# Performance work log

Hardware: AMD Instinct MI355X
Metric: run time of the kernel (lower is better)

## Reference

```python
import jax, jax.numpy as jnp
import numpy as np
from jax import lax

HEADS, HEAD_DIM, DIM, DIM_OUT, EPS = 12, 64, 768, 768, 1e-5
REL_DIM = 2 * 56 - 1  # 2*max(q_size, kv_size) - 1


def setup_inputs():
    key = jax.random.key(0)
    ks = jax.random.split(key, 10)
    B, T, H, W = 4, 1, 56, 56
    N = 1 + T * H * W
    s = 0.02
    return {
        "x": jax.random.normal(ks[0], (B, N, DIM), jnp.float32),
        "Wqkv": jax.random.normal(ks[1], (DIM, 3 * DIM_OUT), jnp.float32) * s,
        "pool_q_w": jax.random.normal(ks[2], (HEAD_DIM, 1, 3, 3), jnp.float32) * 0.1,
        "pool_k_w": jax.random.normal(ks[3], (HEAD_DIM, 1, 3, 3), jnp.float32) * 0.1,
        "pool_v_w": jax.random.normal(ks[4], (HEAD_DIM, 1, 3, 3), jnp.float32) * 0.1,
        "gq": jnp.ones((HEAD_DIM,), jnp.float32), "bq": jnp.zeros((HEAD_DIM,), jnp.float32),
        "gk": jnp.ones((HEAD_DIM,), jnp.float32), "bk": jnp.zeros((HEAD_DIM,), jnp.float32),
        "gv": jnp.ones((HEAD_DIM,), jnp.float32), "bv": jnp.zeros((HEAD_DIM,), jnp.float32),
        "rel_pos_h": jax.random.normal(ks[5], (REL_DIM, HEAD_DIM), jnp.float32) * s,
        "rel_pos_w": jax.random.normal(ks[6], (REL_DIM, HEAD_DIM), jnp.float32) * s,
        "Wproj": jax.random.normal(ks[7], (DIM_OUT, DIM_OUT), jnp.float32) * s,
        "bproj": jnp.zeros((DIM_OUT,), jnp.float32),
        "T": 1, "H": 56, "W": 56,
    }


def _layernorm(y, g, b):
    mu = y.mean(-1, keepdims=True)
    var = ((y - mu) ** 2).mean(-1, keepdims=True)
    return (y - mu) * lax.rsqrt(var + EPS) * g + b


def _pool(t, w, stride, g, b, B, H, W):
    # t: (B, heads, 1 + H*W, head_dim). Split cls, depthwise conv over spatial body.
    cls, body = t[:, :, :1], t[:, :, 1:]
    y = body.reshape(B * HEADS, H, W, HEAD_DIM).transpose(0, 3, 1, 2)  # (BH, C, H, W)
    y = lax.conv_general_dilated(y, w, (stride, stride), [(1, 1), (1, 1)],
                                 feature_group_count=HEAD_DIM,
                                 dimension_numbers=("NCHW", "OIHW", "NCHW"))
    Ho, Wo = y.shape[2], y.shape[3]
    y = y.reshape(B, HEADS, HEAD_DIM, Ho * Wo).transpose(0, 1, 3, 2)
    y = jnp.concatenate([cls, y], axis=2)
    return _layernorm(y, g, b), Ho, Wo


def _forward(x, Wqkv, pool_q_w, pool_k_w, pool_v_w, gq, bq, gk, bk, gv, bv,
             rel_pos_h, rel_pos_w, Wproj, bproj, T, H, W):
    B, N, _ = x.shape
    scale = HEAD_DIM ** -0.5
    qkv = (x @ Wqkv).reshape(B, N, 3, HEADS, HEAD_DIM).transpose(2, 0, 3, 1, 4)
    q, k, v = qkv[0], qkv[1], qkv[2]  # (B, heads, N, head_dim)
    q, q_h, q_w = _pool(q, pool_q_w, 1, gq, bq, B, H, W)
    k, k_h, k_w = _pool(k, pool_k_w, 2, gk, bk, B, H, W)
    v, _, _ = _pool(v, pool_v_w, 2, gv, bv, B, H, W)
    attn = jnp.einsum("bhqd,bhkd->bhqk", q * scale, k)
    # relative position bias; index tables are static (shapes known at trace time)
    dh = (np.arange(q_h)[:, None] * max(k_h / q_h, 1.0)
          - np.arange(k_h)[None, :] * max(q_h / k_h, 1.0)
          + (k_h - 1) * max(q_h / k_h, 1.0)).astype(np.int32)
    dw = (np.arange(q_w)[:, None] * max(k_w / q_w, 1.0)
          - np.arange(k_w)[None, :] * max(q_w / k_w, 1.0)
          + (k_w - 1) * max(q_w / k_w, 1.0)).astype(np.int32)
    Rh, Rw = rel_pos_h[dh], rel_pos_w[dw]  # (q_h, k_h, c), (q_w, k_w, c)
    r_q = q[:, :, 1:].reshape(B, HEADS, q_h, q_w, HEAD_DIM)
    rel_h = jnp.einsum("byhwc,hkc->byhwk", r_q, Rh)
    rel_w = jnp.einsum("byhwc,wkc->byhwk", r_q, Rw)
    body = (attn[:, :, 1:, 1:].reshape(B, HEADS, q_h, q_w, k_h, k_w)
            + rel_h[..., None] + rel_w[..., None, :])
    attn = attn.at[:, :, 1:, 1:].set(body.reshape(B, HEADS, q_h * q_w, k_h * k_w))
    attn = jax.nn.softmax(attn, axis=-1)
    out = attn @ v
    out = out.at[:, :, 1:, :].add(q[:, :, 1:, :])  # residual pooling (skips cls)
    out = out.transpose(0, 2, 1, 3).reshape(B, -1, DIM_OUT)
    return out @ Wproj + bproj


def reference(x, Wqkv, pool_q_w, pool_k_w, pool_v_w, gq, bq, gk, bk, gv, bv,
              rel_pos_h, rel_pos_w, Wproj, bproj, T, H, W):
    return _forward(x, Wqkv, pool_q_w, pool_k_w, pool_v_w, gq, bq, gk, bk, gv, bv,
                    rel_pos_h, rel_pos_w, Wproj, bproj, T, H, W)
```

## Files before the change

kernel.cpp:

```cpp
#include <hip/hip_runtime.h>
#include <hip/hip_bf16.h>

#define BATCH 4
#define NTOK 3137
#define DIM 768
#define NHEAD 12
#define HD 64
#define QH 56
#define QW 56
#define NKEY 785
#define NKEYPAD 800
#define THREE_DIM 2304
#define MROWS (BATCH*NTOK)
#define QTILE 64
#define NQT 50
#define NBH 48
#define RELROWS (NBH*56)
#define XD 128

typedef __attribute__((ext_vector_type(8))) short bf16x8;
typedef __attribute__((ext_vector_type(4))) float f32x4;

__device__ __forceinline__ unsigned short f2bf(float f) {
    union { float f; unsigned u; } v; v.f = f;
    unsigned r = v.u + 0x7FFFu + ((v.u >> 16) & 1u);
    return (unsigned short)(r >> 16);
}
__device__ __forceinline__ float bf2f(unsigned short s) {
    union { unsigned u; float f; } v; v.u = (unsigned)s << 16; return v.f;
}
__device__ __forceinline__ int swz64(int x) { return x ^ (((x >> 6) & 7) << 4); }

__device__ __forceinline__ void gl16(const void* g, void* l) {
    __builtin_amdgcn_global_load_lds(
        (const __attribute__((address_space(1))) unsigned int*)g,
        (__attribute__((address_space(3))) unsigned int*)l, 16, 0, 0);
}

__global__ __launch_bounds__(256) void cvt_bf16(
    const float* __restrict__ in, unsigned short* __restrict__ outp, int n4)
{
    for (int i = blockIdx.x * 256 + threadIdx.x; i < n4; i += gridDim.x * 256) {
        float4 v = reinterpret_cast<const float4*>(in)[i];
        union { unsigned short s[4]; uint2 u; } o;
        o.s[0] = f2bf(v.x); o.s[1] = f2bf(v.y);
        o.s[2] = f2bf(v.z); o.s[3] = f2bf(v.w);
        reinterpret_cast<uint2*>(outp)[i] = o.u;
    }
}

__global__ __launch_bounds__(256) void cvt_rel(
    const float* __restrict__ h, const float* __restrict__ w,
    unsigned short* __restrict__ hb, unsigned short* __restrict__ wb)
{
    int i = blockIdx.x * 256 + threadIdx.x;
    const float* src; unsigned short* dst; int j;
    if (i < 1776)      { src = h; dst = hb; j = i; }
    else if (i < 3552) { src = w; dst = wb; j = i - 1776; }
    else return;
    float4 v = reinterpret_cast<const float4*>(src)[j];
    union { unsigned short s[4]; uint2 u; } o;
    o.s[0] = f2bf(v.x); o.s[1] = f2bf(v.y);
    o.s[2] = f2bf(v.z); o.s[3] = f2bf(v.w);
    reinterpret_cast<uint2*>(dst)[j] = o.u;
}

__global__ __launch_bounds__(256) void transpose_bf16_2(
    const float* __restrict__ W0, unsigned short* __restrict__ Wt0,
    const float* __restrict__ W1, unsigned short* __restrict__ Wt1)
{
    const float* W; unsigned short* Wt; int N;
    if (blockIdx.z == 0) { W = W0; Wt = Wt0; N = THREE_DIM; }
    else {
        if (blockIdx.x >= DIM / 32) return;
        W = W1; Wt = Wt1; N = DIM;
    }
    const int K = DIM;
    __shared__ float tile[32][33];
    int k0 = blockIdx.y * 32, n0 = blockIdx.x * 32;
    int t = threadIdx.x;
    int r = t >> 5, c = t & 31;
    #pragma unroll
    for (int p = 0; p < 4; ++p)
        tile[r + p * 8][c] = W[(size_t)(k0 + r + p * 8) * N + n0 + c];
    __syncthreads();
    #pragma unroll
    for (int p = 0; p < 4; ++p)
        Wt[(size_t)(n0 + r + p * 8) * K + k0 + c] = f2bf(tile[c][r + p * 8]);
}

__global__ __launch_bounds__(256) void gemm_mfma(
    const unsigned short* __restrict__ A, const unsigned short* __restrict__ Bt,
    const float* __restrict__ bias, void* __restrict__ C,
    int M, int N, int K, int out_bf16)
{
    __shared__ __align__(16) char lds[32768];
    int t = threadIdx.x;
    int wave = t >> 6, lane = t & 63;
    int lm = lane & 15, lkg = lane >> 4;
    int wr = wave >> 1, wc = wave & 1;

    int gx = gridDim.x;
    int nwg = gx * gridDim.y;
    int lin = blockIdx.y * gx + blockIdx.x;
    int qq = nwg >> 3, rr = nwg & 7;
    int xcd = lin & 7, idx = lin >> 3;
    int newlin = (xcd < rr ? xcd * (qq + 1) : rr * (qq + 1) + (xcd - rr) * qq) + idx;
    int m0 = (newlin / gx) * 128, n0 = (newlin % gx) * 128;

    int o0 = wave * 2048 + lane * 16;
    int o1 = o0 + 1024;
    int r0 = o0 >> 6, s0 = ((o0 >> 4) & 3) ^ ((r0 >> 1) & 3);
    int r1 = o1 >> 6, s1 = ((o1 >> 4) & 3) ^ ((r1 >> 1) & 3);
    int ar0 = m0 + r0; if (ar0 >= M) ar0 = M - 1;
    int ar1 = m0 + r1; if (ar1 >= M) ar1 = M - 1;

    const unsigned short* ap0 = A + (size_t)ar0 * K + s0 * 8;
    const unsigned short* ap1 = A + (size_t)ar1 * K + s1 * 8;
    const unsigned short* bp0 = Bt + (size_t)(n0 + r0) * K + s0 * 8;
    const unsigned short* bp1 = Bt + (size_t)(n0 + r1) * K + s1 * 8;

    int oa0 = o0, oa1 = o1, ob0 = 8192 + o0, ob1 = 8192 + o1;

    f32x4 acc[4][4] = {};
    const int nt = K >> 5;

    gl16(ap0, &lds[oa0]); gl16(ap1, &lds[oa1]);
    gl16(bp0, &lds[ob0]); gl16(bp1, &lds[ob1]);
    ap0 += 32; ap1 += 32; bp0 += 32; bp1 += 32;

    for (int tt = 0; tt < nt; ++tt) {
        int cb = (tt & 1) << 14;
        if (tt + 1 < nt) {
            int nb2 = cb ^ 16384;
            gl16(ap0, &lds[nb2 + oa0]); gl16(ap1, &lds[nb2 + oa1]);
            gl16(bp0, &lds[nb2 + ob0]); gl16(bp1, &lds[nb2 + ob1]);
            ap0 += 32; ap1 += 32; bp0 += 32; bp1 += 32;
            asm volatile("s_waitcnt vmcnt(4)" ::: "memory");
        } else {
            asm volatile("s_waitcnt vmcnt(0)" ::: "memory");
        }
        __builtin_amdgcn_s_barrier();

        bf16x8 af[4], bfr[4];
        #pragma unroll
        for (int m = 0; m < 4; ++m) {
            int row = wr * 64 + m * 16 + lm;
            af[m] = *reinterpret_cast<const bf16x8*>(
                &lds[cb + row * 64 + ((lkg ^ ((row >> 1) & 3)) << 4)]);
        }
        #pragma unroll
        for (int n = 0; n < 4; ++n) {
            int row = wc * 64 + n * 16 + lm;
            bfr[n] = *reinterpret_cast<const bf16x8*>(
                &lds[cb + 8192 + row * 64 + ((lkg ^ ((row >> 1) & 3)) << 4)]);
        }
        #pragma unroll
        for (int m = 0; m < 4; ++m)
            #pragma unroll
            for (int n = 0; n < 4; ++n)
                acc[m][n] = __builtin_amdgcn_mfma_f32_16x16x32_bf16(
                    af[m], bfr[n], acc[m][n], 0, 0, 0);
        __builtin_amdgcn_s_barrier();
    }

    #pragma unroll
    for (int n = 0; n < 4; ++n) {
        int col = n0 + wc * 64 + n * 16 + lm;
        float bval = bias ? bias[col] : 0.f;
        #pragma unroll
        for (int m = 0; m < 4; ++m) {
            int row = m0 + wr * 64 + m * 16 + lkg * 4;
            #pragma unroll
            for (int r = 0; r < 4; ++r) {
                if (row + r < M) {
                    float o = acc[m][n][r] + bval;
                    if (out_bf16)
                        ((unsigned short*)C)[(size_t)(row + r) * N + col] = f2bf(o);
                    else
                        ((float*)C)[(size_t)(row + r) * N + col] = o;
                }
            }
        }
    }
}

__global__ __launch_bounds__(256) void pool_ln_rows(
    const unsigned short* __restrict__ qkvb, const float* __restrict__ w,
    const float* __restrict__ g, const float* __restrict__ beta,
    unsigned short* __restrict__ outp, int qi, int stride, int OH, int OW,
    int mode)
{
    __shared__ unsigned short ibuf[3 * 56 * 64];
    int bid = blockIdx.x;
    int orow = bid % OH;
    int bh = bid / OH;
    int head = bh % NHEAD, b = bh / NHEAD;
    int t = threadIdx.x;
    int wave = t >> 6, lane = t & 63;

    const unsigned short* src =
        qkvb + (size_t)b * NTOK * THREE_DIM + (size_t)qi * DIM + (size_t)head * HD;

    for (int i = t; i < 3 * 56 * 32; i += 256) {
        int pair = i >> 5, off = i & 31;
        int r = pair / 56, iw = pair % 56;
        int ih = orow * stride + r - 1;
        unsigned v = 0;
        if (ih >= 0 && ih < QH)
            v = *reinterpret_cast<const unsigned*>(
                src + (size_t)(1 + ih * QW + iw) * THREE_DIM + off * 2);
        *reinterpret_cast<unsigned*>(&ibuf[pair * 64 + off * 2]) = v;
    }

    float wreg[9];
    #pragma unroll
    for (int k = 0; k < 9; ++k) wreg[k] = w[lane * 9 + k];
    float gl = g[lane], bl = beta[lane];
    __syncthreads();

    int ntask = OW + ((orow == 0) ? 1 : 0);
    for (int task = wave; task < ntask; task += 4) {
        float val;
        int pos;
        if (task == OW) {
            val = bf2f(src[lane]);
            pos = 0;
        } else {
            int ow = task;
            float acc = 0.f;
            #pragma unroll
            for (int r = 0; r < 3; ++r) {
                #pragma unroll
                for (int c = 0; c < 3; ++c) {
                    int iwc = ow * stride + c - 1;
                    if (iwc < 0 || iwc >= QW) continue;
                    acc += bf2f(ibuf[(r * 56 + iwc) * 64 + lane]) * wreg[r * 3 + c];
                }
            }
            val = acc;
            pos = 1 + orow * OW + ow;
        }

        float mu = val;
        #pragma unroll
        for (int off = 32; off > 0; off >>= 1) mu += __shfl_xor(mu, off, 64);
        mu *= (1.f / 64.f);
        float dv = val - mu;
        float var = dv * dv;
        #pragma unroll
        for (int off = 32; off > 0; off >>= 1) var += __shfl_xor(var, off, 64);
        var *= (1.f / 64.f);
        float o = dv * rsqrtf(var + 1e-5f) * gl + bl;

        if (mode == 3) {
            unsigned short* row = outp + ((size_t)bh * NTOK + pos) * XD;
            row[lane] = f2bf(o * 0.125f);
            row[64 + lane] = (lane == 56) ? f2bf(-30.f) : 0;
        } else if (mode == 1) {
            unsigned short* row = outp + ((size_t)bh * NKEYPAD + pos) * XD;
            row[lane] = f2bf(o);
            unsigned short ext = 0;
            if (pos > 0) {
                int kh = (pos - 1) / 28, kw = (pos - 1) % 28;
                if ((lane < 28 && lane == kh) ||
                    (lane >= 28 && lane < 56 && lane - 28 == kw))
                    ext = 0x3F80;
            }
            row[64 + lane] = ext;
        } else {
            outp[((size_t)bh * HD + lane) * NKEYPAD + pos] = f2bf(o);
        }
    }
}

__global__ __launch_bounds__(64) void pad_kv(
    unsigned short* __restrict__ kpx, unsigned short* __restrict__ vt16)
{
    int bh = blockIdx.x;
    int t = threadIdx.x;
    for (int pos = NKEY; pos < NKEYPAD; ++pos) {
        unsigned short* row = kpx + ((size_t)bh * NKEYPAD + pos) * XD;
        row[t] = 0;
        row[64 + t] = (t == 56) ? 0x3F80 : 0;
        vt16[((size_t)bh * HD + t) * NKEYPAD + pos] = 0;
    }
}

__global__ __launch_bounds__(256) void rel_mfma(
    const unsigned short* __restrict__ qpx, const unsigned short* __restrict__ rtab,
    unsigned short* __restrict__ qpx_out, int mode)
{
    __shared__ char bbuf[4096];
    int X = blockIdx.x;
    int m0 = blockIdx.y * 256;
    int t = threadIdx.x;
    int wave = t >> 6, lane = t & 63;
    int lm = lane & 15, lkg = lane >> 4;

    {
        int row = t >> 3, c8 = t & 7;
        int4 val = {0, 0, 0, 0};
        if (row < 28) {
            int dh = X - 2 * row + 54;
            val = *reinterpret_cast<const int4*>(rtab + (size_t)dh * HD + c8 * 8);
        }
        *reinterpret_cast<int4*>(&bbuf[row * 128 + ((c8 * 16) ^ ((row & 7) << 4))]) = val;
    }
    __syncthreads();

    int rbase = m0 + wave * 64 + lm;
    f32x4 acc[4][2] = {};
    #pragma unroll
    for (int kc = 0; kc < 2; ++kc) {
        bf16x8 bfrag[2];
        #pragma unroll
        for (int nb = 0; nb < 2; ++nb) {
            int row = nb * 16 + lm;
            bfrag[nb] = *reinterpret_cast<const bf16x8*>(
                &bbuf[row * 128 + (((kc * 4 + lkg) * 16) ^ ((row & 7) << 4))]);
        }
        #pragma unroll
        for (int m = 0; m < 4; ++m) {
            int rho = rbase + m * 16; if (rho > RELROWS - 1) rho = RELROWS - 1;
            int bh = rho / 56, rem = rho % 56;
            int pos1 = (mode == 0) ? X * 56 + rem : rem * 56 + X;
            const unsigned short* qsrc =
                qpx + ((size_t)bh * NTOK + 1 + pos1) * XD + kc * 32 + lkg * 8;
            bf16x8 af = *reinterpret_cast<const bf16x8*>(qsrc);
            acc[m][0] = __builtin_amdgcn_mfma_f32_16x16x32_bf16(af, bfrag[0], acc[m][0], 0, 0, 0);
            acc[m][1] = __builtin_amdgcn_mfma_f32_16x16x32_bf16(af, bfrag[1], acc[m][1], 0, 0, 0);
        }
    }

    #pragma unroll
    for (int m = 0; m < 4; ++m) {
        #pragma unroll
        for (int r = 0; r < 4; ++r) {
            int rho = m0 + wave * 64 + m * 16 + lkg * 4 + r;
            if (rho >= RELROWS) continue;
            int bh = rho / 56, rem = rho % 56;
            int pos1 = (mode == 0) ? X * 56 + rem : rem * 56 + X;
            unsigned short* dst =
                qpx_out + ((size_t)bh * NTOK + 1 + pos1) * XD + 64 + mode * 28;
            dst[lm] = f2bf(acc[m][0][r] * 8.f);
            if (lm < 12) dst[16 + lm] = f2bf(acc[m][1][r] * 8.f);
        }
    }
}

__global__ __launch_bounds__(256) void attn_mfma(
    const unsigned short* __restrict__ qpx, const unsigned short* __restrict__ kpx,
    const unsigned short* __restrict__ vt, unsigned short* __restrict__ outp)
{
    __shared__ __align__(16) char kbuf[2][8192];
    __shared__ __align__(16) char vbuf[2][4096];
    __shared__ __align__(16) char pbuf[4][1024];

    int bid0 = blockIdx.x;
    int bid = (bid0 & 7) * ((NBH * NQT) / 8) + (bid0 >> 3);
    int tile = bid % NQT;
    int bh = bid / NQT;
    int head = bh % NHEAD, b = bh / NHEAD;
    int q0 = tile * QTILE;
    int t = threadIdx.x;
    int wave = t >> 6, lane = t & 63;
    int lm = lane & 15, lkg = lane >> 4;

    const unsigned short* kb  = kpx + (size_t)bh * NKEYPAD * XD;
    const unsigned short* vtb = vt + (size_t)bh * HD * NKEYPAD;

    bf16x8 qf[4] = {};
    int qrow = q0 + wave * 16 + lm;
    if (qrow < NTOK) {
        const unsigned short* qs = qpx + ((size_t)bh * NTOK + qrow) * XD + lkg * 8;
        qf[0] = *reinterpret_cast<const bf16x8*>(qs);
        qf[1] = *reinterpret_cast<const bf16x8*>(qs + 32);
        qf[2] = *reinterpret_cast<const bf16x8*>(qs + 64);
        qf[3] = *reinterpret_cast<const bf16x8*>(qs + 96);
    }

    f32x4 oacc[4] = {};
    float osum[4] = {0.f, 0.f, 0.f, 0.f};

    int kr0 = t >> 4;
    int ks0 = (t & 15) ^ (kr0 & 7);
    int kr1 = kr0 + 16;
    const unsigned short* kp0 = kb + (size_t)kr0 * XD + ks0 * 8;
    const unsigned short* kp1 = kb + (size_t)kr1 * XD + ks0 * 8;
    int vr = t >> 2;
    int vs = (t & 3) ^ ((vr >> 1) & 3);
    const unsigned short* vp0 = vtb + (size_t)vr * NKEYPAD + vs * 8;
    int kd0 = wave * 1024, kd1 = 4096 + wave * 1024, vd = wave * 1024;

    const int NT = NKEYPAD / 32;

    gl16(kp0, &kbuf[0][kd0]); gl16(kp1, &kbuf[0][kd1]); gl16(vp0, &vbuf[0][vd]);
    kp0 += 32 * XD; kp1 += 32 * XD; vp0 += 32;

    for (int jt = 0; jt < NT; ++jt) {
        int cur = jt & 1;
        if (jt + 1 < NT) {
            gl16(kp0, &kbuf[cur ^ 1][kd0]);
            gl16(kp1, &kbuf[cur ^ 1][kd1]);
            gl16(vp0, &vbuf[cur ^ 1][vd]);
            kp0 += 32 * XD; kp1 += 32 * XD; vp0 += 32;
            asm volatile("s_waitcnt vmcnt(3)" ::: "memory");
        } else {
            asm volatile("s_waitcnt vmcnt(0)" ::: "memory");
        }
        __builtin_amdgcn_s_barrier();

        f32x4 acc0 = {0.f, 0.f, 0.f, 0.f}, acc1 = {0.f, 0.f, 0.f, 0.f};
        #pragma unroll
        for (int kc = 0; kc < 4; ++kc) {
            int sl = (kc * 4 + lkg) ^ (lm & 7);
            bf16x8 kf0 = *reinterpret_cast<const bf16x8*>(&kbuf[cur][lm * 256 + sl * 16]);
            acc0 = __builtin_amdgcn_mfma_f32_16x16x32_bf16(qf[kc], kf0, acc0, 0, 0, 0);
            bf16x8 kf1 = *reinterpret_cast<const bf16x8*>(&kbuf[cur][(16 + lm) * 256 + sl * 16]);
            acc1 = __builtin_amdgcn_mfma_f32_16x16x32_bf16(qf[kc], kf1, acc1, 0, 0, 0);
        }

        #pragma unroll
        for (int nb = 0; nb < 2; ++nb) {
            f32x4 a = nb ? acc1 : acc0;
            #pragma unroll
            for (int r = 0; r < 4; ++r) {
                float e = __expf(a[r]);
                osum[r] += e;
                int baddr = (lkg * 4 + r) * 64 + (nb * 16 + lm) * 2;
                *reinterpret_cast<unsigned short*>(&pbuf[wave][swz64(baddr)]) = f2bf(e);
            }
        }

        bf16x8 pf = *reinterpret_cast<const bf16x8*>(&pbuf[wave][swz64(lm * 64 + lkg * 16)]);
        #pragma unroll
        for (int db = 0; db < 4; ++db) {
            int row = db * 16 + lm;
            bf16x8 vf = *reinterpret_cast<const bf16x8*>(
                &vbuf[cur][row * 64 + ((lkg ^ ((row >> 1) & 3)) << 4)]);
            oacc[db] = __builtin_amdgcn_mfma_f32_16x16x32_bf16(pf, vf, oacc[db], 0, 0, 0);
        }

        __builtin_amdgcn_s_barrier();
    }

    #pragma unroll
    for (int r = 0; r < 4; ++r) {
        float s = osum[r];
        s += __shfl_xor(s, 1, 64);
        s += __shfl_xor(s, 2, 64);
        s += __shfl_xor(s, 4, 64);
        s += __shfl_xor(s, 8, 64);
        osum[r] = 1.f / s;
    }
    #pragma unroll
    for (int r = 0; r < 4; ++r) {
        int qpos = q0 + wave * 16 + lkg * 4 + r;
        if (qpos >= NTOK) continue;
        unsigned short* orow = outp + ((size_t)b * NTOK + qpos) * DIM + (size_t)head * HD;
        const unsigned short* qres = qpx + ((size_t)bh * NTOK + qpos) * XD;
        #pragma unroll
        for (int db = 0; db < 4; ++db) {
            int d = db * 16 + lm;
            float o = oacc[db][r] * osum[r];
            if (qpos > 0) o += bf2f(qres[d]) * 8.f;
            orow[d] = f2bf(o);
        }
    }
}

extern "C" void kernel_launch(void* const* d_in, const int* in_sizes, int n_in,
                              void* d_out, int out_size, void* d_ws, size_t ws_size,
                              hipStream_t stream) {
    const float* x     = (const float*)d_in[0];
    const float* Wqkv  = (const float*)d_in[1];
    const float* pqw   = (const float*)d_in[2];
    const float* pkw   = (const float*)d_in[3];
    const float* pvw   = (const float*)d_in[4];
    const float* gq    = (const float*)d_in[5];
    const float* bq    = (const float*)d_in[6];
    const float* gk    = (const float*)d_in[7];
    const float* bk    = (const float*)d_in[8];
    const float* gv    = (const float*)d_in[9];
    const float* bv    = (const float*)d_in[10];
    const float* rph   = (const float*)d_in[11];
    const float* rpw   = (const float*)d_in[12];
    const float* Wproj = (const float*)d_in[13];
    const float* bproj = (const float*)d_in[14];

    unsigned short* qkvb  = (unsigned short*)d_ws;
    unsigned short* qpx   = qkvb + (size_t)MROWS * THREE_DIM;
    unsigned short* kpx   = qpx + (size_t)NBH * NTOK * XD;
    unsigned short* vt16  = kpx + (size_t)NBH * NKEYPAD * XD;
    unsigned short* xbf   = vt16 + (size_t)NBH * HD * NKEYPAD;
    unsigned short* wqkvt = xbf + (size_t)MROWS * DIM;
    unsigned short* wprojt= wqkvt + (size_t)DIM * THREE_DIM;
    unsigned short* rphb  = wprojt + (size_t)DIM * DIM;
    unsigned short* rpwb  = rphb + 7104;
    unsigned short* attn_bf = qkvb;

    dim3 blk(256);

    cvt_bf16<<<2048, blk, 0, stream>>>(x, xbf, (int)((size_t)MROWS * DIM / 4));
    {
        dim3 g(THREE_DIM / 32, DIM / 32, 2);
        transpose_bf16_2<<<g, blk, 0, stream>>>(Wqkv, wqkvt, Wproj, wprojt);
    }
    cvt_rel<<<14, blk, 0, stream>>>(rph, rpw, rphb, rpwb);

    {
        dim3 grid(THREE_DIM / 128, (MROWS + 127) / 128);
        gemm_mfma<<<grid, blk, 0, stream>>>(xbf, wqkvt, nullptr, qkvb,
                                            MROWS, THREE_DIM, DIM, 1);
    }

    pool_ln_rows<<<NBH * QH, blk, 0, stream>>>(qkvb, pqw, gq, bq, qpx,  0, 1, QH, QW, 3);
    pool_ln_rows<<<NBH * 28, blk, 0, stream>>>(qkvb, pkw, gk, bk, kpx,  1, 2, 28, 28, 1);
    pool_ln_rows<<<NBH * 28, blk, 0, stream>>>(qkvb, pvw, gv, bv, vt16, 2, 2, 28, 28, 2);
    pad_kv<<<NBH, 64, 0, stream>>>(kpx, vt16);

    {
        dim3 g(56, (RELROWS + 255) / 256);
        rel_mfma<<<g, blk, 0, stream>>>(qpx, rphb, qpx, 0);
        rel_mfma<<<g, blk, 0, stream>>>(qpx, rpwb, qpx, 1);
    }

    attn_mfma<<<NBH * NQT, blk, 0, stream>>>(qpx, kpx, vt16, attn_bf);

    {
        dim3 grid(DIM / 128, (MROWS + 127) / 128);
        gemm_mfma<<<grid, blk, 0, stream>>>(attn_bf, wprojt, bproj, d_out,
                                            MROWS, DIM, DIM, 0);
    }
}
```

Before: 329.4 us.

## Use 256x256 triple-buffered GEMM tiles and triple-buffer attention K/V loads

```diff
diff --git a/kernel.cpp b/kernel.cpp
--- a/kernel.cpp
+++ b/kernel.cpp
@@ -89,16 +89,16 @@
         Wt[(size_t)(n0 + r + p * 8) * K + k0 + c] = f2bf(tile[c][r + p * 8]);
 }
 
-__global__ __launch_bounds__(256) void gemm_mfma(
+__global__ __launch_bounds__(512, 2) void gemm_mfma256(
     const unsigned short* __restrict__ A, const unsigned short* __restrict__ Bt,
     const float* __restrict__ bias, void* __restrict__ C,
     int M, int N, int K, int out_bf16)
 {
-    __shared__ __align__(16) char lds[32768];
+    __shared__ __align__(16) char lds[98304];
     int t = threadIdx.x;
     int wave = t >> 6, lane = t & 63;
     int lm = lane & 15, lkg = lane >> 4;
-    int wr = wave >> 1, wc = wave & 1;
+    int wr = wave >> 2, wc = wave & 3;
 
     int gx = gridDim.x;
     int nwg = gx * gridDim.y;
@@ -106,62 +106,76 @@
     int qq = nwg >> 3, rr = nwg & 7;
     int xcd = lin & 7, idx = lin >> 3;
     int newlin = (xcd < rr ? xcd * (qq + 1) : rr * (qq + 1) + (xcd - rr) * qq) + idx;
-    int m0 = (newlin / gx) * 128, n0 = (newlin % gx) * 128;
-
-    int o0 = wave * 2048 + lane * 16;
-    int o1 = o0 + 1024;
-    int r0 = o0 >> 6, s0 = ((o0 >> 4) & 3) ^ ((r0 >> 1) & 3);
-    int r1 = o1 >> 6, s1 = ((o1 >> 4) & 3) ^ ((r1 >> 1) & 3);
-    int ar0 = m0 + r0; if (ar0 >= M) ar0 = M - 1;
-    int ar1 = m0 + r1; if (ar1 >= M) ar1 = M - 1;
-
-    const unsigned short* ap0 = A + (size_t)ar0 * K + s0 * 8;
-    const unsigned short* ap1 = A + (size_t)ar1 * K + s1 * 8;
-    const unsigned short* bp0 = Bt + (size_t)(n0 + r0) * K + s0 * 8;
-    const unsigned short* bp1 = Bt + (size_t)(n0 + r1) * K + s1 * 8;
-
-    int oa0 = o0, oa1 = o1, ob0 = 8192 + o0, ob1 = 8192 + o1;
-
-    f32x4 acc[4][4] = {};
+    int m0 = (newlin / gx) * 256, n0 = (newlin % gx) * 256;
+
+    const unsigned short* gp0; const unsigned short* gp1;
+    const unsigned short* gp2; const unsigned short* gp3;
+    int lo0, lo1, lo2, lo3;
+    {
+        int o, ob, row, slot, r;
+        o = 0 * 8192 + t * 16; ob = o; row = ob >> 6;
+        slot = ((ob >> 4) & 3) ^ ((row >> 1) & 3);
+        r = m0 + row; if (r >= M) r = M - 1;
+        gp0 = A + (size_t)r * K + slot * 8; lo0 = o;
+
+        o = 1 * 8192 + t * 16; ob = o; row = ob >> 6;
+        slot = ((ob >> 4) & 3) ^ ((row >> 1) & 3);
+        r = m0 + row; if (r >= M) r = M - 1;
+        gp1 = A + (size_t)r * K + slot * 8; lo1 = o;
+
+        o = 2 * 8192 + t * 16; ob = o - 16384; row = ob >> 6;
+        slot = ((ob >> 4) & 3) ^ ((row >> 1) & 3);
+        gp2 = Bt + (size_t)(n0 + row) * K + slot * 8; lo2 = o;
+
+        o = 3 * 8192 + t * 16; ob = o - 16384; row = ob >> 6;
+        slot = ((ob >> 4) & 3) ^ ((row >> 1) & 3);
+        gp3 = Bt + (size_t)(n0 + row) * K + slot * 8; lo3 = o;
+    }
+
+    f32x4 acc[8][4] = {};
     const int nt = K >> 5;
 
-    gl16(ap0, &lds[oa0]); gl16(ap1, &lds[oa1]);
-    gl16(bp0, &lds[ob0]); gl16(bp1, &lds[ob1]);
-    ap0 += 32; ap1 += 32; bp0 += 32; bp1 += 32;
-
+    gl16(gp0, &lds[lo0]); gl16(gp1, &lds[lo1]);
+    gl16(gp2, &lds[lo2]); gl16(gp3, &lds[lo3]);
+    gp0 += 32; gp1 += 32; gp2 += 32; gp3 += 32;
+    gl16(gp0, &lds[32768 + lo0]); gl16(gp1, &lds[32768 + lo1]);
+    gl16(gp2, &lds[32768 + lo2]); gl16(gp3, &lds[32768 + lo3]);
+    gp0 += 32; gp1 += 32; gp2 += 32; gp3 += 32;
+
+    int cur = 0;
     for (int tt = 0; tt < nt; ++tt) {
-        int cb = (tt & 1) << 14;
-        if (tt + 1 < nt) {
-            int nb2 = cb ^ 16384;
-            gl16(ap0, &lds[nb2 + oa0]); gl16(ap1, &lds[nb2 + oa1]);
-            gl16(bp0, &lds[nb2 + ob0]); gl16(bp1, &lds[nb2 + ob1]);
-            ap0 += 32; ap1 += 32; bp0 += 32; bp1 += 32;
-            asm volatile("s_waitcnt vmcnt(4)" ::: "memory");
-        } else {
-            asm volatile("s_waitcnt vmcnt(0)" ::: "memory");
-        }
+        if (tt + 1 < nt) asm volatile("s_waitcnt vmcnt(4)" ::: "memory");
+        else             asm volatile("s_waitcnt vmcnt(0)" ::: "memory");
         __builtin_amdgcn_s_barrier();
 
-        bf16x8 af[4], bfr[4];
-        #pragma unroll
-        for (int m = 0; m < 4; ++m) {
-            int row = wr * 64 + m * 16 + lm;
+        char* base = &lds[cur << 15];
+        bf16x8 af[8], bfr[4];
+        #pragma unroll
+        for (int m = 0; m < 8; ++m) {
+            int row = wr * 128 + m * 16 + lm;
             af[m] = *reinterpret_cast<const bf16x8*>(
-                &lds[cb + row * 64 + ((lkg ^ ((row >> 1) & 3)) << 4)]);
+                base + row * 64 + ((lkg ^ ((row >> 1) & 3)) << 4));
         }
         #pragma unroll
         for (int n = 0; n < 4; ++n) {
             int row = wc * 64 + n * 16 + lm;
             bfr[n] = *reinterpret_cast<const bf16x8*>(
-                &lds[cb + 8192 + row * 64 + ((lkg ^ ((row >> 1) & 3)) << 4)]);
-        }
-        #pragma unroll
-        for (int m = 0; m < 4; ++m)
+                base + 16384 + row * 64 + ((lkg ^ ((row >> 1) & 3)) << 4));
+        }
+        if (tt + 2 < nt) {
+            int nx = cur + 2; if (nx >= 3) nx -= 3;
+            char* nb = &lds[nx << 15];
+            gl16(gp0, nb + lo0); gl16(gp1, nb + lo1);
+            gl16(gp2, nb + lo2); gl16(gp3, nb + lo3);
+            gp0 += 32; gp1 += 32; gp2 += 32; gp3 += 32;
+        }
+        #pragma unroll
+        for (int m = 0; m < 8; ++m)
             #pragma unroll
             for (int n = 0; n < 4; ++n)
                 acc[m][n] = __builtin_amdgcn_mfma_f32_16x16x32_bf16(
                     af[m], bfr[n], acc[m][n], 0, 0, 0);
-        __builtin_amdgcn_s_barrier();
+        cur = (cur == 2) ? 0 : cur + 1;
     }
 
     #pragma unroll
@@ -169,16 +183,16 @@
         int col = n0 + wc * 64 + n * 16 + lm;
         float bval = bias ? bias[col] : 0.f;
         #pragma unroll
-        for (int m = 0; m < 4; ++m) {
-            int row = m0 + wr * 64 + m * 16 + lkg * 4;
+        for (int m = 0; m < 8; ++m) {
+            int rowb = m0 + wr * 128 + m * 16 + lkg * 4;
             #pragma unroll
             for (int r = 0; r < 4; ++r) {
-                if (row + r < M) {
+                if (rowb + r < M) {
                     float o = acc[m][n][r] + bval;
                     if (out_bf16)
-                        ((unsigned short*)C)[(size_t)(row + r) * N + col] = f2bf(o);
+                        ((unsigned short*)C)[(size_t)(rowb + r) * N + col] = f2bf(o);
                     else
-                        ((float*)C)[(size_t)(row + r) * N + col] = o;
+                        ((float*)C)[(size_t)(rowb + r) * N + col] = o;
                 }
             }
         }
@@ -353,8 +367,8 @@
     const unsigned short* __restrict__ qpx, const unsigned short* __restrict__ kpx,
     const unsigned short* __restrict__ vt, unsigned short* __restrict__ outp)
 {
-    __shared__ __align__(16) char kbuf[2][8192];
-    __shared__ __align__(16) char vbuf[2][4096];
+    __shared__ __align__(16) char kbuf[3][8192];
+    __shared__ __align__(16) char vbuf[3][4096];
     __shared__ __align__(16) char pbuf[4][1024];
 
     int bid0 = blockIdx.x;
@@ -397,18 +411,13 @@
 
     gl16(kp0, &kbuf[0][kd0]); gl16(kp1, &kbuf[0][kd1]); gl16(vp0, &vbuf[0][vd]);
     kp0 += 32 * XD; kp1 += 32 * XD; vp0 += 32;
-
+    gl16(kp0, &kbuf[1][kd0]); gl16(kp1, &kbuf[1][kd1]); gl16(vp0, &vbuf[1][vd]);
+    kp0 += 32 * XD; kp1 += 32 * XD; vp0 += 32;
+
+    int cur = 0;
     for (int jt = 0; jt < NT; ++jt) {
-        int cur = jt & 1;
-        if (jt + 1 < NT) {
-            gl16(kp0, &kbuf[cur ^ 1][kd0]);
-            gl16(kp1, &kbuf[cur ^ 1][kd1]);
-            gl16(vp0, &vbuf[cur ^ 1][vd]);
-            kp0 += 32 * XD; kp1 += 32 * XD; vp0 += 32;
-            asm volatile("s_waitcnt vmcnt(3)" ::: "memory");
-        } else {
-            asm volatile("s_waitcnt vmcnt(0)" ::: "memory");
-        }
+        if (jt + 1 < NT) asm volatile("s_waitcnt vmcnt(3)" ::: "memory");
+        else             asm volatile("s_waitcnt vmcnt(0)" ::: "memory");
         __builtin_amdgcn_s_barrier();
 
         f32x4 acc0 = {0.f, 0.f, 0.f, 0.f}, acc1 = {0.f, 0.f, 0.f, 0.f};
@@ -419,6 +428,14 @@
             acc0 = __builtin_amdgcn_mfma_f32_16x16x32_bf16(qf[kc], kf0, acc0, 0, 0, 0);
             bf16x8 kf1 = *reinterpret_cast<const bf16x8*>(&kbuf[cur][(16 + lm) * 256 + sl * 16]);
             acc1 = __builtin_amdgcn_mfma_f32_16x16x32_bf16(qf[kc], kf1, acc1, 0, 0, 0);
+        }
+
+        if (jt + 2 < NT) {
+            int nx = cur + 2; if (nx >= 3) nx -= 3;
+            gl16(kp0, &kbuf[nx][kd0]);
+            gl16(kp1, &kbuf[nx][kd1]);
+            gl16(vp0, &vbuf[nx][vd]);
+            kp0 += 32 * XD; kp1 += 32 * XD; vp0 += 32;
         }
 
         #pragma unroll
@@ -442,7 +459,7 @@
             oacc[db] = __builtin_amdgcn_mfma_f32_16x16x32_bf16(pf, vf, oacc[db], 0, 0, 0);
         }
 
-        __builtin_amdgcn_s_barrier();
+        cur = (cur == 2) ? 0 : cur + 1;
     }
 
     #pragma unroll
@@ -501,6 +518,7 @@
     unsigned short* attn_bf = qkvb;
 
     dim3 blk(256);
+    dim3 blk512(512);
 
     cvt_bf16<<<2048, blk, 0, stream>>>(x, xbf, (int)((size_t)MROWS * DIM / 4));
     {
@@ -510,9 +528,9 @@
     cvt_rel<<<14, blk, 0, stream>>>(rph, rpw, rphb, rpwb);
 
     {
-        dim3 grid(THREE_DIM / 128, (MROWS + 127) / 128);
-        gemm_mfma<<<grid, blk, 0, stream>>>(xbf, wqkvt, nullptr, qkvb,
-                                            MROWS, THREE_DIM, DIM, 1);
+        dim3 grid(THREE_DIM / 256, (MROWS + 255) / 256);
+        gemm_mfma256<<<grid, blk512, 0, stream>>>(xbf, wqkvt, nullptr, qkvb,
+                                                  MROWS, THREE_DIM, DIM, 1);
     }
 
     pool_ln_rows<<<NBH * QH, blk, 0, stream>>>(qkvb, pqw, gq, bq, qpx,  0, 1, QH, QW, 3);
@@ -529,8 +547,8 @@
     attn_mfma<<<NBH * NQT, blk, 0, stream>>>(qpx, kpx, vt16, attn_bf);
 
     {
-        dim3 grid(DIM / 128, (MROWS + 127) / 128);
-        gemm_mfma<<<grid, blk, 0, stream>>>(attn_bf, wprojt, bproj, d_out,
-                                            MROWS, DIM, DIM, 0);
-    }
-}
+        dim3 grid(DIM / 256, (MROWS + 255) / 256);
+        gemm_mfma256<<<grid, blk512, 0, stream>>>(attn_bf, wprojt, bproj, d_out,
+                                                  MROWS, DIM, DIM, 0);
+    }
+}
```

After: 330.0 us. No clear change (+0.2%).

## Triple-buffer GEMM and attention loads, use exp2 with prescaled Q, merge rel launches

Applied to the files above, without the earlier changes.

```diff
diff --git a/kernel.cpp b/kernel.cpp
--- a/kernel.cpp
+++ b/kernel.cpp
@@ -18,6 +18,10 @@
 #define RELROWS (NBH*56)
 #define XD 128
 
+#define QSCALE 0.1803368801111204f
+#define QUNSCALE 5.5451774444795625f
+#define PADSUP  -43.3f
+
 typedef __attribute__((ext_vector_type(8))) short bf16x8;
 typedef __attribute__((ext_vector_type(4))) float f32x4;
 
@@ -89,12 +93,12 @@
         Wt[(size_t)(n0 + r + p * 8) * K + k0 + c] = f2bf(tile[c][r + p * 8]);
 }
 
-__global__ __launch_bounds__(256) void gemm_mfma(
+__global__ __launch_bounds__(256, 3) void gemm_mfma(
     const unsigned short* __restrict__ A, const unsigned short* __restrict__ Bt,
     const float* __restrict__ bias, void* __restrict__ C,
     int M, int N, int K, int out_bf16)
 {
-    __shared__ __align__(16) char lds[32768];
+    __shared__ __align__(16) char lds[49152];
     int t = threadIdx.x;
     int wave = t >> 6, lane = t & 63;
     int lm = lane & 15, lkg = lane >> 4;
@@ -108,52 +112,57 @@
     int newlin = (xcd < rr ? xcd * (qq + 1) : rr * (qq + 1) + (xcd - rr) * qq) + idx;
     int m0 = (newlin / gx) * 128, n0 = (newlin % gx) * 128;
 
-    int o0 = wave * 2048 + lane * 16;
-    int o1 = o0 + 1024;
-    int r0 = o0 >> 6, s0 = ((o0 >> 4) & 3) ^ ((r0 >> 1) & 3);
-    int r1 = o1 >> 6, s1 = ((o1 >> 4) & 3) ^ ((r1 >> 1) & 3);
-    int ar0 = m0 + r0; if (ar0 >= M) ar0 = M - 1;
-    int ar1 = m0 + r1; if (ar1 >= M) ar1 = M - 1;
-
-    const unsigned short* ap0 = A + (size_t)ar0 * K + s0 * 8;
-    const unsigned short* ap1 = A + (size_t)ar1 * K + s1 * 8;
-    const unsigned short* bp0 = Bt + (size_t)(n0 + r0) * K + s0 * 8;
-    const unsigned short* bp1 = Bt + (size_t)(n0 + r1) * K + s1 * 8;
-
-    int oa0 = o0, oa1 = o1, ob0 = 8192 + o0, ob1 = 8192 + o1;
+    const unsigned short *gpa0, *gpa1, *gpb0, *gpb1;
+    int la0, la1, lb0, lb1;
+    {
+        int o0 = t * 16, o1 = 4096 + t * 16;
+        int r0 = o0 >> 6, s0 = ((o0 >> 4) & 3) ^ ((r0 >> 1) & 3);
+        int r1 = o1 >> 6, s1 = ((o1 >> 4) & 3) ^ ((r1 >> 1) & 3);
+        int ar0 = m0 + r0; if (ar0 >= M) ar0 = M - 1;
+        int ar1 = m0 + r1; if (ar1 >= M) ar1 = M - 1;
+        gpa0 = A + (size_t)ar0 * K + s0 * 8;  la0 = o0;
+        gpa1 = A + (size_t)ar1 * K + s1 * 8;  la1 = o1;
+        gpb0 = Bt + (size_t)(n0 + r0) * K + s0 * 8;  lb0 = 8192 + o0;
+        gpb1 = Bt + (size_t)(n0 + r1) * K + s1 * 8;  lb1 = 8192 + o1;
+    }
 
     f32x4 acc[4][4] = {};
     const int nt = K >> 5;
 
-    gl16(ap0, &lds[oa0]); gl16(ap1, &lds[oa1]);
-    gl16(bp0, &lds[ob0]); gl16(bp1, &lds[ob1]);
-    ap0 += 32; ap1 += 32; bp0 += 32; bp1 += 32;
-
+    gl16(gpa0, &lds[la0]); gl16(gpa1, &lds[la1]);
+    gl16(gpb0, &lds[lb0]); gl16(gpb1, &lds[lb1]);
+    gpa0 += 32; gpa1 += 32; gpb0 += 32; gpb1 += 32;
+    gl16(gpa0, &lds[16384 + la0]); gl16(gpa1, &lds[16384 + la1]);
+    gl16(gpb0, &lds[16384 + lb0]); gl16(gpb1, &lds[16384 + lb1]);
+    gpa0 += 32; gpa1 += 32; gpb0 += 32; gpb1 += 32;
+
+    int cur = 0;
     for (int tt = 0; tt < nt; ++tt) {
-        int cb = (tt & 1) << 14;
-        if (tt + 1 < nt) {
-            int nb2 = cb ^ 16384;
-            gl16(ap0, &lds[nb2 + oa0]); gl16(ap1, &lds[nb2 + oa1]);
-            gl16(bp0, &lds[nb2 + ob0]); gl16(bp1, &lds[nb2 + ob1]);
-            ap0 += 32; ap1 += 32; bp0 += 32; bp1 += 32;
-            asm volatile("s_waitcnt vmcnt(4)" ::: "memory");
-        } else {
-            asm volatile("s_waitcnt vmcnt(0)" ::: "memory");
-        }
+        if (tt + 1 < nt) asm volatile("s_waitcnt vmcnt(4)" ::: "memory");
+        else             asm volatile("s_waitcnt vmcnt(0)" ::: "memory");
         __builtin_amdgcn_s_barrier();
 
+        if (tt + 2 < nt) {
+            int nx = cur + 2; if (nx >= 3) nx -= 3;
+            char* nb = &lds[nx << 14];
+            gl16(gpa0, nb + la0); gl16(gpa1, nb + la1);
+            gl16(gpb0, nb + lb0); gl16(gpb1, nb + lb1);
+            gpa0 += 32; gpa1 += 32; gpb0 += 32; gpb1 += 32;
+        }
+
+        char* base = &lds[cur << 14];
         bf16x8 af[4], bfr[4];
         #pragma unroll
         for (int m = 0; m < 4; ++m) {
             int row = wr * 64 + m * 16 + lm;
             af[m] = *reinterpret_cast<const bf16x8*>(
-                &lds[cb + row * 64 + ((lkg ^ ((row >> 1) & 3)) << 4)]);
+                base + row * 64 + ((lkg ^ ((row >> 1) & 3)) << 4));
         }
         #pragma unroll
         for (int n = 0; n < 4; ++n) {
             int row = wc * 64 + n * 16 + lm;
             bfr[n] = *reinterpret_cast<const bf16x8*>(
-                &lds[cb + 8192 + row * 64 + ((lkg ^ ((row >> 1) & 3)) << 4)]);
+                base + 8192 + row * 64 + ((lkg ^ ((row >> 1) & 3)) << 4));
         }
         #pragma unroll
         for (int m = 0; m < 4; ++m)
@@ -161,25 +170,28 @@
             for (int n = 0; n < 4; ++n)
                 acc[m][n] = __builtin_amdgcn_mfma_f32_16x16x32_bf16(
                     af[m], bfr[n], acc[m][n], 0, 0, 0);
-        __builtin_amdgcn_s_barrier();
-    }
-
-    #pragma unroll
-    for (int n = 0; n < 4; ++n) {
-        int col = n0 + wc * 64 + n * 16 + lm;
-        float bval = bias ? bias[col] : 0.f;
-        #pragma unroll
-        for (int m = 0; m < 4; ++m) {
-            int row = m0 + wr * 64 + m * 16 + lkg * 4;
+
+        cur = (cur == 2) ? 0 : cur + 1;
+    }
+
+    float bv[4];
+    #pragma unroll
+    for (int n = 0; n < 4; ++n)
+        bv[n] = bias ? bias[n0 + wc * 64 + n * 16 + lm] : 0.f;
+    #pragma unroll
+    for (int m = 0; m < 4; ++m) {
+        #pragma unroll
+        for (int r = 0; r < 4; ++r) {
+            int row = m0 + wr * 64 + m * 16 + lkg * 4 + r;
+            if (row >= M) continue;
             #pragma unroll
-            for (int r = 0; r < 4; ++r) {
-                if (row + r < M) {
-                    float o = acc[m][n][r] + bval;
-                    if (out_bf16)
-                        ((unsigned short*)C)[(size_t)(row + r) * N + col] = f2bf(o);
-                    else
-                        ((float*)C)[(size_t)(row + r) * N + col] = o;
-                }
+            for (int n = 0; n < 4; ++n) {
+                int col = n0 + wc * 64 + n * 16 + lm;
+                float o = acc[m][n][r] + bv[n];
+                if (out_bf16)
+                    ((unsigned short*)C)[(size_t)row * N + col] = f2bf(o);
+                else
+                    ((float*)C)[(size_t)row * N + col] = o;
             }
         }
     }
@@ -255,8 +267,8 @@
 
         if (mode == 3) {
             unsigned short* row = outp + ((size_t)bh * NTOK + pos) * XD;
-            row[lane] = f2bf(o * 0.125f);
-            row[64 + lane] = (lane == 56) ? f2bf(-30.f) : 0;
+            row[lane] = f2bf(o * QSCALE);
+            row[64 + lane] = (lane == 56) ? f2bf(PADSUP) : 0;
         } else if (mode == 1) {
             unsigned short* row = outp + ((size_t)bh * NKEYPAD + pos) * XD;
             row[lane] = f2bf(o);
@@ -288,12 +300,14 @@
 }
 
 __global__ __launch_bounds__(256) void rel_mfma(
-    const unsigned short* __restrict__ qpx, const unsigned short* __restrict__ rtab,
-    unsigned short* __restrict__ qpx_out, int mode)
+    const unsigned short* __restrict__ qpx, const unsigned short* __restrict__ rh,
+    const unsigned short* __restrict__ rw, unsigned short* __restrict__ qpx_out)
 {
     __shared__ char bbuf[4096];
     int X = blockIdx.x;
     int m0 = blockIdx.y * 256;
+    int mode = blockIdx.z;
+    const unsigned short* rtab = mode ? rw : rh;
     int t = threadIdx.x;
     int wave = t >> 6, lane = t & 63;
     int lm = lane & 15, lkg = lane >> 4;
@@ -353,8 +367,8 @@
     const unsigned short* __restrict__ qpx, const unsigned short* __restrict__ kpx,
     const unsigned short* __restrict__ vt, unsigned short* __restrict__ outp)
 {
-    __shared__ __align__(16) char kbuf[2][8192];
-    __shared__ __align__(16) char vbuf[2][4096];
+    __shared__ __align__(16) char kbuf[3][8192];
+    __shared__ __align__(16) char vbuf[3][4096];
     __shared__ __align__(16) char pbuf[4][1024];
 
     int bid0 = blockIdx.x;
@@ -397,18 +411,13 @@
 
     gl16(kp0, &kbuf[0][kd0]); gl16(kp1, &kbuf[0][kd1]); gl16(vp0, &vbuf[0][vd]);
     kp0 += 32 * XD; kp1 += 32 * XD; vp0 += 32;
-
+    gl16(kp0, &kbuf[1][kd0]); gl16(kp1, &kbuf[1][kd1]); gl16(vp0, &vbuf[1][vd]);
+    kp0 += 32 * XD; kp1 += 32 * XD; vp0 += 32;
+
+    int cur = 0;
     for (int jt = 0; jt < NT; ++jt) {
-        int cur = jt & 1;
-        if (jt + 1 < NT) {
-            gl16(kp0, &kbuf[cur ^ 1][kd0]);
-            gl16(kp1, &kbuf[cur ^ 1][kd1]);
-            gl16(vp0, &vbuf[cur ^ 1][vd]);
-            kp0 += 32 * XD; kp1 += 32 * XD; vp0 += 32;
-            asm volatile("s_waitcnt vmcnt(3)" ::: "memory");
-        } else {
-            asm volatile("s_waitcnt vmcnt(0)" ::: "memory");
-        }
+        if (jt + 1 < NT) asm volatile("s_waitcnt vmcnt(3)" ::: "memory");
+        else             asm volatile("s_waitcnt vmcnt(0)" ::: "memory");
         __builtin_amdgcn_s_barrier();
 
         f32x4 acc0 = {0.f, 0.f, 0.f, 0.f}, acc1 = {0.f, 0.f, 0.f, 0.f};
@@ -421,15 +430,26 @@
             acc1 = __builtin_amdgcn_mfma_f32_16x16x32_bf16(qf[kc], kf1, acc1, 0, 0, 0);
         }
 
+        if (jt + 2 < NT) {
+            int nx = cur + 2; if (nx >= 3) nx -= 3;
+            gl16(kp0, &kbuf[nx][kd0]);
+            gl16(kp1, &kbuf[nx][kd1]);
+            gl16(vp0, &vbuf[nx][vd]);
+            kp0 += 32 * XD; kp1 += 32 * XD; vp0 += 32;
+        }
+
         #pragma unroll
         for (int nb = 0; nb < 2; ++nb) {
             f32x4 a = nb ? acc1 : acc0;
             #pragma unroll
             for (int r = 0; r < 4; ++r) {
-                float e = __expf(a[r]);
+                float e;
+                asm("v_exp_f32 %0, %1" : "=v"(e) : "v"(a[r]));
                 osum[r] += e;
+                union { float f; unsigned u; } ue; ue.f = e;
                 int baddr = (lkg * 4 + r) * 64 + (nb * 16 + lm) * 2;
-                *reinterpret_cast<unsigned short*>(&pbuf[wave][swz64(baddr)]) = f2bf(e);
+                *reinterpret_cast<unsigned short*>(&pbuf[wave][swz64(baddr)]) =
+                    (unsigned short)(ue.u >> 16);
             }
         }
 
@@ -442,7 +462,7 @@
             oacc[db] = __builtin_amdgcn_mfma_f32_16x16x32_bf16(pf, vf, oacc[db], 0, 0, 0);
         }
 
-        __builtin_amdgcn_s_barrier();
+        cur = (cur == 2) ? 0 : cur + 1;
     }
 
     #pragma unroll
@@ -464,7 +484,7 @@
         for (int db = 0; db < 4; ++db) {
             int d = db * 16 + lm;
             float o = oacc[db][r] * osum[r];
-            if (qpos > 0) o += bf2f(qres[d]) * 8.f;
+            if (qpos > 0) o += bf2f(qres[d]) * QUNSCALE;
             orow[d] = f2bf(o);
         }
     }
@@ -521,9 +541,8 @@
     pad_kv<<<NBH, 64, 0, stream>>>(kpx, vt16);
 
     {
-        dim3 g(56, (RELROWS + 255) / 256);
-        rel_mfma<<<g, blk, 0, stream>>>(qpx, rphb, qpx, 0);
-        rel_mfma<<<g, blk, 0, stream>>>(qpx, rpwb, qpx, 1);
+        dim3 g(56, (RELROWS + 255) / 256, 2);
+        rel_mfma<<<g, blk, 0, stream>>>(qpx, rphb, rpwb, qpx);
     }
 
     attn_mfma<<<NBH * NQT, blk, 0, stream>>>(qpx, kpx, vt16, attn_bf);
```

After: 295.2 us. 10.4% less time.
